# Performance work log

Measured on AMD Instinct MI355X. Metric: run time of the kernel, lower is better.

## Reference

```python
import jax, jax.numpy as jnp
import numpy as np

B, H, S, D = 4, 16, 2048, 128

def setup_inputs() -> dict:
    key = jax.random.key(0)
    kq, kk, kv = jax.random.split(key, 3)
    q = jax.random.normal(kq, (B, H, S, D), dtype=jnp.float32)
    k = jax.random.normal(kk, (B, H, S, D), dtype=jnp.float32)
    v = jax.random.normal(kv, (B, H, S, D), dtype=jnp.float32)
    return {"q": q, "k": k, "v": v}

def reference(q, k, v):
    # NOTE: original module applies NO 1/sqrt(d) scale.
    scores = jnp.einsum("bhqd,bhkd->bhqk", q, k)          # [B,H,S,S]
    weights = jax.nn.softmax(scores, axis=-1)
    return jnp.einsum("bhqk,bhkd->bhqd", weights, v)       # [B,H,S,D]
```

## Files before the change

### kernel.cpp

```cpp
#include <hip/hip_runtime.h>
#include <hip/hip_bf16.h>
#include <math.h>
#include <stdint.h>

#define S_LEN 2048
#define D_DIM 128

typedef _Float16 f16x8 __attribute__((ext_vector_type(8)));
typedef __fp16  fp16x2 __attribute__((ext_vector_type(2)));
typedef short bf8_t __attribute__((ext_vector_type(8)));
typedef float f32x4 __attribute__((ext_vector_type(4)));
typedef _Float16 f16_t;

__device__ __forceinline__ short f2bf(float f) {
    union { float f; unsigned u; } x; x.f = f;
    unsigned u = x.u;
    u += 0x7FFF + ((u >> 16) & 1);
    return (short)(u >> 16);
}
__device__ __forceinline__ float bf2f(short h) {
    union { unsigned u; float f; } x;
    x.u = ((unsigned)(unsigned short)h) << 16;
    return x.f;
}
__device__ __forceinline__ uint32_t pkf16(float a, float b) {
    union { fp16x2 h; uint32_t u; } x;
    x.h = __builtin_amdgcn_cvt_pkrtz(a, b);
    return x.u;
}

#define TILE_B 16384
#define WS_VT  33554432u
#define WS_NEED 67108864u

typedef const uint32_t __attribute__((address_space(1))) ga_u32;
typedef uint32_t __attribute__((address_space(3))) la_u32;
__device__ __forceinline__ void gload16(void* l, const void* g) {
    __builtin_amdgcn_global_load_lds((ga_u32*)g, (la_u32*)l, 16, 0, 0);
}

__global__ __launch_bounds__(256, 4)
void conv_kv(const float* __restrict__ K, const float* __restrict__ V,
             char* __restrict__ kf, char* __restrict__ vt)
{
    size_t tile = blockIdx.x;
    const float4* kg = (const float4*)(K + tile * (64 * 128));
    char* kd = kf + tile * TILE_B;
    #pragma unroll
    for (int it = 0; it < 8; ++it) {
        int idx = it * 256 + threadIdx.x;
        int row = idx >> 5;
        int d0  = (idx & 31) * 4;
        float4 kk = kg[idx];
        uint32_t a = pkf16(kk.x, kk.y);
        uint32_t b = pkf16(kk.z, kk.w);
        uint32_t byte = (uint32_t)((row * 256 + d0 * 2) ^ ((row & 7) << 4));
        *(uint32_t*)(kd + byte)     = a;
        *(uint32_t*)(kd + byte + 4) = b;
    }
    const float* vs = V + tile * (64 * 128);
    char* vd = vt + tile * TILE_B;
    #pragma unroll
    for (int it = 0; it < 8; ++it) {
        int idx = it * 256 + threadIdx.x;
        int d  = idx & 127;
        int k0 = (idx >> 7) * 4;
        uint32_t a = pkf16(vs[(k0 + 0) * 128 + d], vs[(k0 + 1) * 128 + d]);
        uint32_t b = pkf16(vs[(k0 + 2) * 128 + d], vs[(k0 + 3) * 128 + d]);
        uint32_t byte = (uint32_t)((d * 128 + k0 * 2) ^ ((d & 7) << 4));
        *(uint32_t*)(vd + byte)     = a;
        *(uint32_t*)(vd + byte + 4) = b;
    }
}

__global__ __launch_bounds__(512, 4)
void attn_f16(const float* __restrict__ Q, const char* __restrict__ ws,
              float* __restrict__ O)
{
    __shared__ __align__(16) char lds[65536];

    const int tid  = threadIdx.x;
    const int w    = tid >> 6;
    const int lane = tid & 63;
    const int lg   = lane & 15;
    const int gq   = lane >> 4;

    const int fid  = blockIdx.x;
    const int nid  = (fid & 7) * 128 + (fid >> 3);
    const int qblk = nid & 15;
    const int bh   = nid >> 4;

    const size_t base = (size_t)bh * S_LEN * D_DIM;
    const int qrow0 = qblk * 128 + w * 16;

    f16x8 qf[4];
    {
        const float* qp = Q + base + (size_t)(qrow0 + lg) * D_DIM;
        #pragma unroll
        for (int c = 0; c < 4; ++c) {
            #pragma unroll
            for (int jj = 0; jj < 2; ++jj) {
                float4 f = *(const float4*)(qp + c * 32 + gq * 8 + jj * 4);
                qf[c][jj * 4 + 0] = (f16_t)f.x;
                qf[c][jj * 4 + 1] = (f16_t)f.y;
                qf[c][jj * 4 + 2] = (f16_t)f.z;
                qf[c][jj * 4 + 3] = (f16_t)f.w;
            }
        }
    }

    f32x4 oacc[8];
    #pragma unroll
    for (int n = 0; n < 8; ++n) oacc[n] = (f32x4){0.f, 0.f, 0.f, 0.f};
    float m_run = -INFINITY, l_run = 0.f;

    const char* kf_t = ws + (size_t)(bh * 32) * TILE_B;
    const char* vt_t = ws + WS_VT + (size_t)(bh * 32) * TILE_B;
    const int sw = (lg & 7) << 4;

    #pragma unroll
    for (int j = 0; j < 2; ++j) {
        const int off = j * 8192 + w * 1024;
        gload16(lds + off,         kf_t + off + lane * 16);
        gload16(lds + 16384 + off, vt_t + off + lane * 16);
    }
    __syncthreads();

    int bo = 0;
    for (int t6 = 0; t6 < 32; ++t6) {
        if (t6 < 31) {
            const char* kn = kf_t + (size_t)(t6 + 1) * TILE_B;
            const char* vn = vt_t + (size_t)(t6 + 1) * TILE_B;
            const int ob = bo ^ 32768;
            #pragma unroll
            for (int j = 0; j < 2; ++j) {
                const int off = j * 8192 + w * 1024;
                gload16(lds + ob + off,         kn + off + lane * 16);
                gload16(lds + ob + 16384 + off, vn + off + lane * 16);
            }
        }

        f32x4 sacc[4];
        #pragma unroll
        for (int t = 0; t < 4; ++t) sacc[t] = (f32x4){0.f, 0.f, 0.f, 0.f};
        __builtin_amdgcn_s_setprio(1);
        #pragma unroll
        for (int t = 0; t < 4; ++t) {
            const int rb = (t * 16 + lg) * 256;
            #pragma unroll
            for (int c = 0; c < 4; ++c) {
                const int byte = (rb + c * 64 + gq * 16) ^ sw;
                f16x8 kff = *(const f16x8*)(lds + bo + byte);
                sacc[t] = __builtin_amdgcn_mfma_f32_16x16x32_f16(kff, qf[c], sacc[t], 0, 0, 0);
            }
        }
        __builtin_amdgcn_s_setprio(0);

        float tm = sacc[0][0];
        #pragma unroll
        for (int t = 0; t < 4; ++t)
            #pragma unroll
            for (int r = 0; r < 4; ++r) tm = fmaxf(tm, sacc[t][r]);
        tm = fmaxf(tm, __shfl_xor(tm, 16));
        tm = fmaxf(tm, __shfl_xor(tm, 32));
        const int grow = (tm > m_run + 8.f) ? 1 : 0;
        if (__any(grow)) {
            const float mn = fmaxf(m_run, tm);
            const float sc = __expf(m_run - mn);
            m_run = mn;
            l_run *= sc;
            float scq[4];
            #pragma unroll
            for (int r = 0; r < 4; ++r) scq[r] = __shfl(sc, gq * 4 + r);
            #pragma unroll
            for (int n = 0; n < 8; ++n) {
                oacc[n][0] *= scq[0]; oacc[n][1] *= scq[1];
                oacc[n][2] *= scq[2]; oacc[n][3] *= scq[3];
            }
        }
        float ps = 0.f;
        #pragma unroll
        for (int t = 0; t < 4; ++t)
            #pragma unroll
            for (int r = 0; r < 4; ++r) {
                float p = __expf(sacc[t][r] - m_run);
                sacc[t][r] = p;
                ps += p;
            }
        ps += __shfl_xor(ps, 16);
        ps += __shfl_xor(ps, 32);
        l_run += ps;

        uint32_t dw[4][2];
        #pragma unroll
        for (int t = 0; t < 4; ++t) {
            dw[t][0] = pkf16(sacc[t][0], sacc[t][1]);
            dw[t][1] = pkf16(sacc[t][2], sacc[t][3]);
        }
        const int tclass = gq >> 1;
        const int sgl = (2 * (gq & 1)) * 16 + lg;
        #pragma unroll
        for (int kt = 0; kt < 2; ++kt) {
            uint32_t paw[4];
            #pragma unroll
            for (int wd = 0; wd < 4; ++wd) {
                const int src = sgl + (wd >> 1) * 16;
                uint32_t vA = (uint32_t)__shfl((int)dw[2 * kt][wd & 1], src);
                uint32_t vB = (uint32_t)__shfl((int)dw[2 * kt + 1][wd & 1], src);
                paw[wd] = tclass ? vB : vA;
            }
            union { uint32_t u[4]; f16x8 v; } pu;
            pu.u[0] = paw[0]; pu.u[1] = paw[1]; pu.u[2] = paw[2]; pu.u[3] = paw[3];
            f16x8 pa = pu.v;
            __builtin_amdgcn_s_setprio(1);
            #pragma unroll
            for (int n = 0; n < 8; ++n) {
                const int byte = ((n * 16 + lg) * 128 + kt * 64 + gq * 16) ^ sw;
                f16x8 vb = *(const f16x8*)(lds + bo + 16384 + byte);
                oacc[n] = __builtin_amdgcn_mfma_f32_16x16x32_f16(pa, vb, oacc[n], 0, 0, 0);
            }
            __builtin_amdgcn_s_setprio(0);
        }

        __syncthreads();
        bo ^= 32768;
    }

    const float inv_own = 1.f / l_run;
    float invq[4];
    #pragma unroll
    for (int r = 0; r < 4; ++r) invq[r] = __shfl(inv_own, gq * 4 + r);
    float* op = O + base + (size_t)qrow0 * D_DIM;
    #pragma unroll
    for (int n = 0; n < 8; ++n)
        #pragma unroll
        for (int r = 0; r < 4; ++r)
            op[(size_t)(gq * 4 + r) * D_DIM + n * 16 + lg] = oacc[n][r] * invq[r];
}

#define PADK 136
#define PADV 72
#define LDS_SHORTS 31232

__global__ __launch_bounds__(256, 2)
void attn_fwd_fb(const float* __restrict__ Q, const float* __restrict__ K,
                 const float* __restrict__ V, float* __restrict__ O)
{
    __shared__ short lds[LDS_SHORTS];
    short* khi = lds;
    short* klo = lds + 8704;
    short* vt  = lds + 17408;
    short* pls = lds + 26624;

    const int tid  = threadIdx.x;
    const int w    = tid >> 6;
    const int lane = tid & 63;
    const int lg   = lane & 15;
    const int gq   = lane >> 4;
    const int qblk = blockIdx.x;
    const int bh   = blockIdx.y;
    const size_t base = (size_t)bh * S_LEN * D_DIM;
    const int qrow0 = qblk * 64 + w * 16;

    bf8_t qhi[4], qlo[4];
    {
        const float* qp = Q + base + (size_t)(qrow0 + lg) * D_DIM;
        #pragma unroll
        for (int c = 0; c < 4; ++c) {
            const int d0 = c * 32 + gq * 8;
            #pragma unroll
            for (int j = 0; j < 8; ++j) {
                float f = qp[d0 + j];
                short h = f2bf(f);
                qhi[c][j] = h;
                qlo[c][j] = f2bf(f - bf2f(h));
            }
        }
    }

    f32x4 oacc[8];
    #pragma unroll
    for (int n = 0; n < 8; ++n) oacc[n] = (f32x4){0.f, 0.f, 0.f, 0.f};
    float mrow[4] = {-INFINITY, -INFINITY, -INFINITY, -INFINITY};
    float lrow[4] = {0.f, 0.f, 0.f, 0.f};

    for (int kv = 0; kv < S_LEN; kv += 64) {
        __syncthreads();
        {
            const float4* kg = (const float4*)(K + base + (size_t)kv * D_DIM);
            const float4* vg = (const float4*)(V + base + (size_t)kv * D_DIM);
            #pragma unroll
            for (int it = 0; it < 8; ++it) {
                const int f4  = it * 256 + tid;
                const int row = f4 >> 5;
                const int d   = (f4 & 31) * 4;
                float4 kk = kg[f4];
                float4 vv = vg[f4];
                short h0 = f2bf(kk.x), h1 = f2bf(kk.y), h2 = f2bf(kk.z), h3 = f2bf(kk.w);
                short4 hw; hw.x = h0; hw.y = h1; hw.z = h2; hw.w = h3;
                *(short4*)(&khi[row * PADK + d]) = hw;
                short4 lw;
                lw.x = f2bf(kk.x - bf2f(h0));
                lw.y = f2bf(kk.y - bf2f(h1));
                lw.z = f2bf(kk.z - bf2f(h2));
                lw.w = f2bf(kk.w - bf2f(h3));
                *(short4*)(&klo[row * PADK + d]) = lw;
                vt[(d + 0) * PADV + row] = f2bf(vv.x);
                vt[(d + 1) * PADV + row] = f2bf(vv.y);
                vt[(d + 2) * PADV + row] = f2bf(vv.z);
                vt[(d + 3) * PADV + row] = f2bf(vv.w);
            }
        }
        __syncthreads();

        f32x4 sacc[4];
        #pragma unroll
        for (int t = 0; t < 4; ++t) sacc[t] = (f32x4){0.f, 0.f, 0.f, 0.f};
        #pragma unroll
        for (int t = 0; t < 4; ++t) {
            const int krow = t * 16 + lg;
            #pragma unroll
            for (int c = 0; c < 4; ++c) {
                bf8_t kh = *(const bf8_t*)(&khi[krow * PADK + c * 32 + gq * 8]);
                bf8_t kl = *(const bf8_t*)(&klo[krow * PADK + c * 32 + gq * 8]);
                sacc[t] = __builtin_amdgcn_mfma_f32_16x16x32_bf16(qhi[c], kh, sacc[t], 0, 0, 0);
                sacc[t] = __builtin_amdgcn_mfma_f32_16x16x32_bf16(qlo[c], kh, sacc[t], 0, 0, 0);
                sacc[t] = __builtin_amdgcn_mfma_f32_16x16x32_bf16(qhi[c], kl, sacc[t], 0, 0, 0);
            }
        }

        float scl[4];
        #pragma unroll
        for (int r = 0; r < 4; ++r) {
            float tm = fmaxf(fmaxf(sacc[0][r], sacc[1][r]),
                             fmaxf(sacc[2][r], sacc[3][r]));
            #pragma unroll
            for (int off = 8; off >= 1; off >>= 1)
                tm = fmaxf(tm, __shfl_xor(tm, off, 64));
            const float mn = fmaxf(mrow[r], tm);
            const float sc = __expf(mrow[r] - mn);
            float ps = 0.f;
            #pragma unroll
            for (int t = 0; t < 4; ++t) {
                float p = __expf(sacc[t][r] - mn);
                sacc[t][r] = p;
                ps += p;
            }
            #pragma unroll
            for (int off = 8; off >= 1; off >>= 1)
                ps += __shfl_xor(ps, off, 64);
            lrow[r] = lrow[r] * sc + ps;
            mrow[r] = mn;
            scl[r] = sc;
        }
        #pragma unroll
        for (int n = 0; n < 8; ++n) {
            oacc[n][0] *= scl[0];
            oacc[n][1] *= scl[1];
            oacc[n][2] *= scl[2];
            oacc[n][3] *= scl[3];
        }

        short* pw = pls + w * (16 * PADV);
        #pragma unroll
        for (int t = 0; t < 4; ++t)
            #pragma unroll
            for (int r = 0; r < 4; ++r)
                pw[(gq * 4 + r) * PADV + t * 16 + lg] = f2bf(sacc[t][r]);
        asm volatile("s_waitcnt lgkmcnt(0)" ::: "memory");

        #pragma unroll
        for (int kt = 0; kt < 2; ++kt) {
            bf8_t pa = *(const bf8_t*)(&pw[lg * PADV + kt * 32 + gq * 8]);
            #pragma unroll
            for (int n = 0; n < 8; ++n) {
                bf8_t vb = *(const bf8_t*)(&vt[(n * 16 + lg) * PADV + kt * 32 + gq * 8]);
                oacc[n] = __builtin_amdgcn_mfma_f32_16x16x32_bf16(pa, vb, oacc[n], 0, 0, 0);
            }
        }
    }

    float inv[4];
    #pragma unroll
    for (int r = 0; r < 4; ++r) inv[r] = 1.f / lrow[r];
    float* op = O + base + (size_t)qrow0 * D_DIM;
    #pragma unroll
    for (int n = 0; n < 8; ++n)
        #pragma unroll
        for (int r = 0; r < 4; ++r)
            op[(size_t)(gq * 4 + r) * D_DIM + n * 16 + lg] = oacc[n][r] * inv[r];
}

extern "C" void kernel_launch(void* const* d_in, const int* in_sizes, int n_in,
                              void* d_out, int out_size, void* d_ws, size_t ws_size,
                              hipStream_t stream) {
    const float* q = (const float*)d_in[0];
    const float* k = (const float*)d_in[1];
    const float* v = (const float*)d_in[2];
    float* o = (float*)d_out;
    if (ws_size >= (size_t)WS_NEED) {
        char* ws = (char*)d_ws;
        conv_kv<<<2048, 256, 0, stream>>>(k, v, ws, ws + WS_VT);
        attn_f16<<<1024, 512, 0, stream>>>(q, ws, o);
    } else {
        attn_fwd_fb<<<dim3(32, 64), 256, 0, stream>>>(q, k, v, o);
    }
}
```

Baseline: 255.0 us.

## Switch attention kernel to 32x32x16 MFMA with 32-row waves and permlane32 swaps

Rewrites the fp16 flash-attention kernel so each wave handles 32 query rows using 32x32x16 MFMA tiles instead of 16x16x32, with 4 waves per 256-thread block instead of 8 waves per 512. The softmax row reductions and the P-matrix relayout now use permlane32_swap instead of multiple ds shuffles. The aim is fewer LDS reads per FLOP, since larger MFMA tiles reuse each loaded operand more, and cheaper cross-lane exchanges. In exchange each wave keeps more accumulator registers live, and occupancy drops to fewer waves per CU.

```diff
diff --git a/kernel.cpp b/kernel.cpp
--- a/kernel.cpp
+++ b/kernel.cpp
@@ -10,6 +10,8 @@
 typedef __fp16  fp16x2 __attribute__((ext_vector_type(2)));
 typedef short bf8_t __attribute__((ext_vector_type(8)));
 typedef float f32x4 __attribute__((ext_vector_type(4)));
+typedef float f32x16 __attribute__((ext_vector_type(16)));
+typedef unsigned int uint32x2 __attribute__((ext_vector_type(2)));
 typedef _Float16 f16_t;
 
 __device__ __forceinline__ short f2bf(float f) {
@@ -27,6 +29,9 @@
     union { fp16x2 h; uint32_t u; } x;
     x.h = __builtin_amdgcn_cvt_pkrtz(a, b);
     return x.u;
+}
+__device__ __forceinline__ uint32x2 plswap(uint32_t a, uint32_t b) {
+    return __builtin_amdgcn_permlane32_swap(a, b, false, false);
 }
 
 #define TILE_B 16384
@@ -73,17 +78,17 @@
     }
 }
 
-__global__ __launch_bounds__(512, 4)
-void attn_f16(const float* __restrict__ Q, const char* __restrict__ ws,
-              float* __restrict__ O)
+__global__ __launch_bounds__(256, 2)
+void attn32(const float* __restrict__ Q, const char* __restrict__ ws,
+            float* __restrict__ O)
 {
     __shared__ __align__(16) char lds[65536];
 
     const int tid  = threadIdx.x;
     const int w    = tid >> 6;
     const int lane = tid & 63;
-    const int lg   = lane & 15;
-    const int gq   = lane >> 4;
+    const int ql   = lane & 31;
+    const int h    = lane >> 5;
 
     const int fid  = blockIdx.x;
     const int nid  = (fid & 7) * 128 + (fid >> 3);
@@ -91,36 +96,37 @@
     const int bh   = nid >> 4;
 
     const size_t base = (size_t)bh * S_LEN * D_DIM;
-    const int qrow0 = qblk * 128 + w * 16;
-
-    f16x8 qf[4];
+    const int qrow0 = qblk * 128 + w * 32;
+
+    f16x8 qf[8];
     {
-        const float* qp = Q + base + (size_t)(qrow0 + lg) * D_DIM;
-        #pragma unroll
-        for (int c = 0; c < 4; ++c) {
-            #pragma unroll
-            for (int jj = 0; jj < 2; ++jj) {
-                float4 f = *(const float4*)(qp + c * 32 + gq * 8 + jj * 4);
-                qf[c][jj * 4 + 0] = (f16_t)f.x;
-                qf[c][jj * 4 + 1] = (f16_t)f.y;
-                qf[c][jj * 4 + 2] = (f16_t)f.z;
-                qf[c][jj * 4 + 3] = (f16_t)f.w;
-            }
-        }
-    }
-
-    f32x4 oacc[8];
-    #pragma unroll
-    for (int n = 0; n < 8; ++n) oacc[n] = (f32x4){0.f, 0.f, 0.f, 0.f};
+        const float* qp = Q + base + (size_t)(qrow0 + ql) * D_DIM;
+        #pragma unroll
+        for (int c = 0; c < 8; ++c) {
+            const int d0 = c * 16 + h * 8;
+            float4 f0 = *(const float4*)(qp + d0);
+            float4 f1 = *(const float4*)(qp + d0 + 4);
+            qf[c][0] = (f16_t)f0.x; qf[c][1] = (f16_t)f0.y;
+            qf[c][2] = (f16_t)f0.z; qf[c][3] = (f16_t)f0.w;
+            qf[c][4] = (f16_t)f1.x; qf[c][5] = (f16_t)f1.y;
+            qf[c][6] = (f16_t)f1.z; qf[c][7] = (f16_t)f1.w;
+        }
+    }
+
+    f32x16 oacc[4];
+    #pragma unroll
+    for (int nt = 0; nt < 4; ++nt)
+        #pragma unroll
+        for (int r = 0; r < 16; ++r) oacc[nt][r] = 0.f;
     float m_run = -INFINITY, l_run = 0.f;
 
     const char* kf_t = ws + (size_t)(bh * 32) * TILE_B;
     const char* vt_t = ws + WS_VT + (size_t)(bh * 32) * TILE_B;
-    const int sw = (lg & 7) << 4;
-
-    #pragma unroll
-    for (int j = 0; j < 2; ++j) {
-        const int off = j * 8192 + w * 1024;
+    const int sw = (ql & 7) << 4;
+
+    #pragma unroll
+    for (int j = 0; j < 4; ++j) {
+        const int off = j * 4096 + w * 1024;
         gload16(lds + off,         kf_t + off + lane * 16);
         gload16(lds + 16384 + off, vt_t + off + lane * 16);
     }
@@ -133,109 +139,110 @@
             const char* vn = vt_t + (size_t)(t6 + 1) * TILE_B;
             const int ob = bo ^ 32768;
             #pragma unroll
-            for (int j = 0; j < 2; ++j) {
-                const int off = j * 8192 + w * 1024;
+            for (int j = 0; j < 4; ++j) {
+                const int off = j * 4096 + w * 1024;
                 gload16(lds + ob + off,         kn + off + lane * 16);
                 gload16(lds + ob + 16384 + off, vn + off + lane * 16);
             }
         }
 
-        f32x4 sacc[4];
-        #pragma unroll
-        for (int t = 0; t < 4; ++t) sacc[t] = (f32x4){0.f, 0.f, 0.f, 0.f};
+        f32x16 s0, s1;
+        #pragma unroll
+        for (int r = 0; r < 16; ++r) { s0[r] = 0.f; s1[r] = 0.f; }
         __builtin_amdgcn_s_setprio(1);
         #pragma unroll
-        for (int t = 0; t < 4; ++t) {
-            const int rb = (t * 16 + lg) * 256;
-            #pragma unroll
-            for (int c = 0; c < 4; ++c) {
-                const int byte = (rb + c * 64 + gq * 16) ^ sw;
-                f16x8 kff = *(const f16x8*)(lds + bo + byte);
-                sacc[t] = __builtin_amdgcn_mfma_f32_16x16x32_f16(kff, qf[c], sacc[t], 0, 0, 0);
-            }
+        for (int c = 0; c < 8; ++c) {
+            const int b0 = (ql * 256 + c * 32 + h * 16) ^ sw;
+            f16x8 a0 = *(const f16x8*)(lds + bo + b0);
+            f16x8 a1 = *(const f16x8*)(lds + bo + b0 + 8192);
+            s0 = __builtin_amdgcn_mfma_f32_32x32x16_f16(a0, qf[c], s0, 0, 0, 0);
+            s1 = __builtin_amdgcn_mfma_f32_32x32x16_f16(a1, qf[c], s1, 0, 0, 0);
         }
         __builtin_amdgcn_s_setprio(0);
 
-        float tm = sacc[0][0];
-        #pragma unroll
-        for (int t = 0; t < 4; ++t)
-            #pragma unroll
-            for (int r = 0; r < 4; ++r) tm = fmaxf(tm, sacc[t][r]);
-        tm = fmaxf(tm, __shfl_xor(tm, 16));
-        tm = fmaxf(tm, __shfl_xor(tm, 32));
-        const int grow = (tm > m_run + 8.f) ? 1 : 0;
-        if (__any(grow)) {
+        float tm = s0[0];
+        #pragma unroll
+        for (int r = 0; r < 16; ++r) { tm = fmaxf(tm, s0[r]); tm = fmaxf(tm, s1[r]); }
+        {
+            uint32x2 ts = plswap(__float_as_uint(tm), __float_as_uint(tm));
+            tm = fmaxf(__uint_as_float(ts[0]), __uint_as_float(ts[1]));
+        }
+        if (__any(tm > m_run + 8.f)) {
             const float mn = fmaxf(m_run, tm);
             const float sc = __expf(m_run - mn);
             m_run = mn;
             l_run *= sc;
-            float scq[4];
-            #pragma unroll
-            for (int r = 0; r < 4; ++r) scq[r] = __shfl(sc, gq * 4 + r);
-            #pragma unroll
-            for (int n = 0; n < 8; ++n) {
-                oacc[n][0] *= scq[0]; oacc[n][1] *= scq[1];
-                oacc[n][2] *= scq[2]; oacc[n][3] *= scq[3];
+            #pragma unroll
+            for (int r = 0; r < 16; ++r) {
+                const float scq = __shfl(sc, (r & 3) + 8 * (r >> 2) + 4 * h);
+                oacc[0][r] *= scq; oacc[1][r] *= scq;
+                oacc[2][r] *= scq; oacc[3][r] *= scq;
             }
         }
         float ps = 0.f;
         #pragma unroll
-        for (int t = 0; t < 4; ++t)
-            #pragma unroll
-            for (int r = 0; r < 4; ++r) {
-                float p = __expf(sacc[t][r] - m_run);
-                sacc[t][r] = p;
-                ps += p;
-            }
-        ps += __shfl_xor(ps, 16);
-        ps += __shfl_xor(ps, 32);
+        for (int r = 0; r < 16; ++r) {
+            float p0 = __expf(s0[r] - m_run); s0[r] = p0; ps += p0;
+            float p1 = __expf(s1[r] - m_run); s1[r] = p1; ps += p1;
+        }
+        {
+            uint32x2 pss = plswap(__float_as_uint(ps), __float_as_uint(ps));
+            ps = __uint_as_float(pss[0]) + __uint_as_float(pss[1]);
+        }
         l_run += ps;
 
-        uint32_t dw[4][2];
-        #pragma unroll
-        for (int t = 0; t < 4; ++t) {
-            dw[t][0] = pkf16(sacc[t][0], sacc[t][1]);
-            dw[t][1] = pkf16(sacc[t][2], sacc[t][3]);
-        }
-        const int tclass = gq >> 1;
-        const int sgl = (2 * (gq & 1)) * 16 + lg;
-        #pragma unroll
-        for (int kt = 0; kt < 2; ++kt) {
-            uint32_t paw[4];
-            #pragma unroll
-            for (int wd = 0; wd < 4; ++wd) {
-                const int src = sgl + (wd >> 1) * 16;
-                uint32_t vA = (uint32_t)__shfl((int)dw[2 * kt][wd & 1], src);
-                uint32_t vB = (uint32_t)__shfl((int)dw[2 * kt + 1][wd & 1], src);
-                paw[wd] = tclass ? vB : vA;
-            }
-            union { uint32_t u[4]; f16x8 v; } pu;
-            pu.u[0] = paw[0]; pu.u[1] = paw[1]; pu.u[2] = paw[2]; pu.u[3] = paw[3];
-            f16x8 pa = pu.v;
-            __builtin_amdgcn_s_setprio(1);
-            #pragma unroll
-            for (int n = 0; n < 8; ++n) {
-                const int byte = ((n * 16 + lg) * 128 + kt * 64 + gq * 16) ^ sw;
+        f16x8 pf[4];
+        {
+            uint32_t pk[8];
+            #pragma unroll
+            for (int i = 0; i < 8; ++i) pk[i] = pkf16(s0[2 * i], s0[2 * i + 1]);
+            uint32x2 r02 = plswap(pk[0], pk[2]), r13 = plswap(pk[1], pk[3]);
+            uint32x2 r46 = plswap(pk[4], pk[6]), r57 = plswap(pk[5], pk[7]);
+            union { uint32_t u[4]; f16x8 v; } b0, b1;
+            b0.u[0] = r02[0]; b0.u[1] = r13[0]; b0.u[2] = r02[1]; b0.u[3] = r13[1];
+            b1.u[0] = r46[0]; b1.u[1] = r57[0]; b1.u[2] = r46[1]; b1.u[3] = r57[1];
+            pf[0] = b0.v; pf[1] = b1.v;
+        }
+        {
+            uint32_t pk[8];
+            #pragma unroll
+            for (int i = 0; i < 8; ++i) pk[i] = pkf16(s1[2 * i], s1[2 * i + 1]);
+            uint32x2 r02 = plswap(pk[0], pk[2]), r13 = plswap(pk[1], pk[3]);
+            uint32x2 r46 = plswap(pk[4], pk[6]), r57 = plswap(pk[5], pk[7]);
+            union { uint32_t u[4]; f16x8 v; } b0, b1;
+            b0.u[0] = r02[0]; b0.u[1] = r13[0]; b0.u[2] = r02[1]; b0.u[3] = r13[1];
+            b1.u[0] = r46[0]; b1.u[1] = r57[0]; b1.u[2] = r46[1]; b1.u[3] = r57[1];
+            pf[2] = b0.v; pf[3] = b1.v;
+        }
+
+        __builtin_amdgcn_s_setprio(1);
+        #pragma unroll
+        for (int nt = 0; nt < 4; ++nt) {
+            const int rb = (nt * 32 + ql) * 128;
+            #pragma unroll
+            for (int kc = 0; kc < 4; ++kc) {
+                const int byte = (rb + kc * 32 + h * 16) ^ sw;
                 f16x8 vb = *(const f16x8*)(lds + bo + 16384 + byte);
-                oacc[n] = __builtin_amdgcn_mfma_f32_16x16x32_f16(pa, vb, oacc[n], 0, 0, 0);
-            }
-            __builtin_amdgcn_s_setprio(0);
-        }
+                oacc[nt] = __builtin_amdgcn_mfma_f32_32x32x16_f16(pf[kc], vb, oacc[nt], 0, 0, 0);
+            }
+        }
+        __builtin_amdgcn_s_setprio(0);
 
         __syncthreads();
         bo ^= 32768;
     }
 
-    const float inv_own = 1.f / l_run;
-    float invq[4];
-    #pragma unroll
-    for (int r = 0; r < 4; ++r) invq[r] = __shfl(inv_own, gq * 4 + r);
-    float* op = O + base + (size_t)qrow0 * D_DIM;
-    #pragma unroll
-    for (int n = 0; n < 8; ++n)
-        #pragma unroll
-        for (int r = 0; r < 4; ++r)
-            op[(size_t)(gq * 4 + r) * D_DIM + n * 16 + lg] = oacc[n][r] * invq[r];
+    const float inv = 1.f / l_run;
+    #pragma unroll
+    for (int r = 0; r < 16; ++r) {
+        const int qr = (r & 3) + 8 * (r >> 2) + 4 * h;
+        const float iv = __shfl(inv, qr);
+        float* op = O + base + (size_t)(qrow0 + qr) * D_DIM + ql;
+        op[0]  = oacc[0][r] * iv;
+        op[32] = oacc[1][r] * iv;
+        op[64] = oacc[2][r] * iv;
+        op[96] = oacc[3][r] * iv;
+    }
 }
 
 #define PADK 136
@@ -271,9 +278,9 @@
             #pragma unroll
             for (int j = 0; j < 8; ++j) {
                 float f = qp[d0 + j];
-                short h = f2bf(f);
-                qhi[c][j] = h;
-                qlo[c][j] = f2bf(f - bf2f(h));
+                short hh = f2bf(f);
+                qhi[c][j] = hh;
+                qlo[c][j] = f2bf(f - bf2f(hh));
             }
         }
     }
@@ -401,7 +408,7 @@
     if (ws_size >= (size_t)WS_NEED) {
         char* ws = (char*)d_ws;
         conv_kv<<<2048, 256, 0, stream>>>(k, v, ws, ws + WS_VT);
-        attn_f16<<<1024, 512, 0, stream>>>(q, ws, o);
+        attn32<<<1024, 256, 0, stream>>>(q, ws, o);
     } else {
         attn_fwd_fb<<<dim3(32, 64), 256, 0, stream>>>(q, k, v, o);
     }
```

New measurement: 221.9 us. -13.0%, faster.
